# Kernel tuning notes

Measured on AMD Instinct MI355X. Metric: run time of the kernel, lower is better.

The kernel has to match this reference:

```python
import jax, jax.numpy as jnp
import numpy as np

N, C, E = 50000, 64, 800000
EPS = 1e-5

def _ln(h, g, b):
    mu = jnp.mean(h, axis=-1, keepdims=True)
    var = jnp.var(h, axis=-1, keepdims=True)
    return (h - mu) * jax.lax.rsqrt(var + EPS) * g + b

def setup_inputs() -> dict:
    key = jax.random.key(0)
    ks = jax.random.split(key, 16)
    def w(k, i, o):
        return jax.random.normal(k, (i, o), jnp.float32) * (1.0 / np.sqrt(i))
    return {
        "x": jax.random.normal(ks[0], (N, C), jnp.float32),
        "edge_index": jax.random.randint(ks[1], (2, E), 0, N, jnp.int32),
        # structure_predictor: Linear(2C,256) -> LN(256) -> GELU -> Dropout(eval) -> Linear(256,1)
        "sp_w1": w(ks[2], 2 * C, 256), "sp_b1": jnp.zeros((256,), jnp.float32),
        "sp_g": jnp.ones((256,), jnp.float32), "sp_be": jnp.zeros((256,), jnp.float32),
        "sp_w2": w(ks[3], 256, 1), "sp_b2": jnp.zeros((1,), jnp.float32),
        # feature_reconstructor: Linear(C,2C) -> LN(2C) -> GELU -> Dropout(eval) -> Linear(2C,C)
        "fr_w1": w(ks[4], C, 2 * C), "fr_b1": jnp.zeros((2 * C,), jnp.float32),
        "fr_g": jnp.ones((2 * C,), jnp.float32), "fr_be": jnp.zeros((2 * C,), jnp.float32),
        "fr_w2": w(ks[5], 2 * C, C), "fr_b2": jnp.zeros((C,), jnp.float32),
        # projection_head: Linear(C,256) -> LN(256) -> GELU -> Linear(256,128)
        "ph_w1": w(ks[6], C, 256), "ph_b1": jnp.zeros((256,), jnp.float32),
        "ph_g": jnp.ones((256,), jnp.float32), "ph_be": jnp.zeros((256,), jnp.float32),
        "ph_w2": w(ks[7], 256, 128), "ph_b2": jnp.zeros((128,), jnp.float32),
    }

def reference(x, edge_index, sp_w1, sp_b1, sp_g, sp_be, sp_w2, sp_b2,
              fr_w1, fr_b1, fr_g, fr_be, fr_w2, fr_b2,
              ph_w1, ph_b1, ph_g, ph_be, ph_w2, ph_b2):
    row, col = edge_index[0], edge_index[1]
    edge_features = jnp.concatenate([x[row], x[col]], axis=1)  # [E, 2C]
    h = _ln(edge_features @ sp_w1 + sp_b1, sp_g, sp_be)
    structure_pred = jax.nn.gelu(h, approximate=False) @ sp_w2 + sp_b2  # [E, 1]
    h = _ln(x @ fr_w1 + fr_b1, fr_g, fr_be)
    reconstructed = jax.nn.gelu(h, approximate=False) @ fr_w2 + fr_b2  # [N, C]
    h = _ln(x @ ph_w1 + ph_b1, ph_g, ph_be)
    projected = jax.nn.gelu(h, approximate=False) @ ph_w2 + ph_b2  # [N, 128]
    return (structure_pred, reconstructed, projected)
```

## Files before the change

### kernel.cpp

```cpp
#include <hip/hip_runtime.h>
#include <hip/hip_bf16.h>

typedef __attribute__((ext_vector_type(8))) short short8;
typedef __attribute__((ext_vector_type(4))) float f32x4;
typedef __attribute__((ext_vector_type(2))) float f32x2;

#define MFMA(a, b, c) __builtin_amdgcn_mfma_f32_16x16x32_bf16((a), (b), (c), 0, 0, 0)

__device__ __forceinline__ unsigned short f2bf(float f) {
    unsigned int u = __float_as_uint(f);
    u += 0x7fffu + ((u >> 16) & 1u);
    return (unsigned short)(u >> 16);
}

__device__ __forceinline__ unsigned int cvt_pk_bf16(float lo, float hi) {
    unsigned int d;
    asm("v_cvt_pk_bf16_f32 %0, %1, %2" : "=v"(d) : "v"(lo), "v"(hi));
    return d;
}

template<int CTRL>
__device__ __forceinline__ float dpp_addf(float v) {
    int t = __builtin_amdgcn_update_dpp(0, __float_as_int(v), CTRL, 0xF, 0xF, true);
    return v + __int_as_float(t);
}
__device__ __forceinline__ float rowsum16(float v) {
    v = dpp_addf<0x121>(v);
    v = dpp_addf<0x122>(v);
    v = dpp_addf<0x124>(v);
    v = dpp_addf<0x128>(v);
    return v;
}

#if __has_builtin(__builtin_amdgcn_exp2f)
#define EXP2(x) __builtin_amdgcn_exp2f(x)
#else
#define EXP2(x) __expf((x) * 0.69314718f)
#endif

__device__ __forceinline__ float gelu_fast(float x) {
    float a = x * __builtin_fmaf(x * x, 0.10295427f, 2.3021210f);
    float E = EXP2(a);
    float r = __builtin_amdgcn_rcpf(E + 1.0f);
    return __builtin_fmaf(-x, r, x);
}

__device__ __forceinline__ f32x2 gelu_fast2(f32x2 x) {
    f32x2 c1 = {2.3021210f, 2.3021210f}, c2 = {0.10295427f, 0.10295427f};
    f32x2 a = x * __builtin_elementwise_fma(x * x, c2, c1);
    f32x2 E;
    E[0] = EXP2(a[0]); E[1] = EXP2(a[1]);
    f32x2 Ep = E + (f32x2){1.f, 1.f};
    f32x2 r;
    r[0] = __builtin_amdgcn_rcpf(Ep[0]); r[1] = __builtin_amdgcn_rcpf(Ep[1]);
    return __builtin_elementwise_fma(-x, r, x);
}

__device__ __forceinline__ f32x2 unpk_bf2(unsigned int a) {
    f32x2 r;
    r[0] = __uint_as_float(a << 16);
    r[1] = __uint_as_float(a & 0xffff0000u);
    return r;
}

__device__ __forceinline__ short8 load_bfrag(const float* __restrict__ w, int k0, int n, int ldn) {
    short8 r;
#pragma unroll
    for (int u = 0; u < 8; ++u)
        r[u] = (short)f2bf(w[(k0 + u) * ldn + n]);
    return r;
}
__device__ __forceinline__ short8 load_bfrag_pk(const unsigned short* __restrict__ wp,
                                                int k0, int n, int krows) {
    return *(const short8*)&wp[(n * (krows >> 3) + (k0 >> 3)) << 3];
}

template<int N1P>
struct SmemMlp {
    unsigned short sS[64 * N1P];
    float rstat[64 * 8];
};

template<int K, int N1, int N2, int MI, bool PK>
__device__ void mlp_tile(SmemMlp<N1 + 8>& sm, const float* __restrict__ x,
                         const void* __restrict__ w1v, const float* __restrict__ b1,
                         const float* __restrict__ g, const float* __restrict__ be,
                         const void* __restrict__ w2v, const float* __restrict__ b2,
                         float* __restrict__ out, int Nrows, int t) {
    constexpr int R = MI * 16;
    constexpr int KP = K + 8, N1P = N1 + 8;
    constexpr int CPW1 = N1 / 4;
    constexpr int JT1 = CPW1 / 16;
    constexpr int KK1 = K / 32;
    constexpr int KK2 = N1 / 32;
    constexpr int JT2 = N2 / 64;
    constexpr int TPR = 256 / R;
    constexpr int FPT = K / TPR;
    constexpr int F4 = FPT / 4;

    const int tid = threadIdx.x;
    const int wave = tid >> 6, lane = tid & 63;
    const int l15 = lane & 15, quad = lane >> 4;
    const int r0 = t * R;

    {
        int m0 = tid / TPR, pp = tid % TPR;
        int rowg = r0 + m0; if (rowg >= Nrows) rowg = Nrows - 1;
        const float4* src = (const float4*)(x + (long)rowg * K + pp * FPT);
        unsigned short* dst = &sm.sS[m0 * KP + pp * FPT];
#pragma unroll
        for (int u = 0; u < F4; ++u) {
            float4 f = src[u];
            ushort4 h; h.x = f2bf(f.x); h.y = f2bf(f.y); h.z = f2bf(f.z); h.w = f2bf(f.w);
            *(ushort4*)(dst + 4 * u) = h;
        }
    }

    short8 breg1[JT1][KK1];
#pragma unroll
    for (int j = 0; j < JT1; ++j)
#pragma unroll
        for (int kk = 0; kk < KK1; ++kk) {
            int k0 = kk * 32 + quad * 8, n = CPW1 * wave + 16 * j + l15;
            if constexpr (PK) breg1[j][kk] = load_bfrag_pk((const unsigned short*)w1v, k0, n, K);
            else              breg1[j][kk] = load_bfrag((const float*)w1v, k0, n, N1);
        }

    float b1v[JT1], gv[JT1], bev[JT1];
#pragma unroll
    for (int j = 0; j < JT1; ++j) {
        int c = CPW1 * wave + 16 * j + l15;
        b1v[j] = b1[c]; gv[j] = g[c]; bev[j] = be[c];
    }
    float b2v[JT2];
#pragma unroll
    for (int j = 0; j < JT2; ++j) b2v[j] = b2[wave * 16 * JT2 + 16 * j + l15];

    __syncthreads();

    f32x4 acc1[MI][JT1];
#pragma unroll
    for (int i = 0; i < MI; ++i)
#pragma unroll
        for (int j = 0; j < JT1; ++j)
            acc1[i][j] = (f32x4){0.f, 0.f, 0.f, 0.f};

#pragma unroll
    for (int kk = 0; kk < KK1; ++kk) {
        short8 a[MI];
#pragma unroll
        for (int i = 0; i < MI; ++i)
            a[i] = *(const short8*)&sm.sS[(16 * i + l15) * KP + kk * 32 + quad * 8];
#pragma unroll
        for (int i = 0; i < MI; ++i)
#pragma unroll
            for (int j = 0; j < JT1; ++j)
                acc1[i][j] = MFMA(a[i], breg1[j][kk], acc1[i][j]);
    }

#pragma unroll
    for (int i = 0; i < MI; ++i)
#pragma unroll
        for (int r = 0; r < 4; ++r) {
            float s = 0.f, ss = 0.f;
#pragma unroll
            for (int j = 0; j < JT1; ++j) {
                float v = acc1[i][j][r] + b1v[j];
                acc1[i][j][r] = v;
                s += v; ss = __builtin_fmaf(v, v, ss);
            }
            s = rowsum16(s); ss = rowsum16(ss);
            if (l15 == 0) {
                int row = 16 * i + quad * 4 + r;
                *(float2*)&sm.rstat[row * 8 + wave * 2] = make_float2(s, ss);
            }
        }
    __syncthreads();

#pragma unroll
    for (int i = 0; i < MI; ++i)
#pragma unroll
        for (int r = 0; r < 4; ++r) {
            int row = 16 * i + quad * 4 + r;
            const float4* st = (const float4*)&sm.rstat[row * 8];
            float4 q0 = st[0], q1 = st[1];
            float s  = (q0.x + q0.z) + (q1.x + q1.z);
            float ss = (q0.y + q0.w) + (q1.y + q1.w);
            float mean = s * (1.f / (float)N1);
            float var  = __builtin_fmaf(ss, 1.f / (float)N1, -mean * mean);
            float rstd = __builtin_amdgcn_rsqf(var + 1e-5f);
            float nm = -mean * rstd;
#pragma unroll
            for (int j = 0; j < JT1; ++j) {
                float tt = __builtin_fmaf(acc1[i][j][r], rstd, nm);
                float xn = __builtin_fmaf(tt, gv[j], bev[j]);
                sm.sS[row * N1P + CPW1 * wave + 16 * j + l15] = f2bf(gelu_fast(xn));
            }
        }
    __syncthreads();

    f32x4 acc2[MI][JT2];
#pragma unroll
    for (int i = 0; i < MI; ++i)
#pragma unroll
        for (int j = 0; j < JT2; ++j)
            acc2[i][j] = (f32x4){0.f, 0.f, 0.f, 0.f};

#pragma unroll
    for (int kk = 0; kk < KK2; ++kk) {
        short8 bf[JT2];
#pragma unroll
        for (int j = 0; j < JT2; ++j) {
            int k0 = kk * 32 + quad * 8, n = wave * 16 * JT2 + 16 * j + l15;
            if constexpr (PK) bf[j] = load_bfrag_pk((const unsigned short*)w2v, k0, n, N1);
            else              bf[j] = load_bfrag((const float*)w2v, k0, n, N2);
        }
        short8 a[MI];
#pragma unroll
        for (int i = 0; i < MI; ++i)
            a[i] = *(const short8*)&sm.sS[(16 * i + l15) * N1P + kk * 32 + quad * 8];
#pragma unroll
        for (int i = 0; i < MI; ++i)
#pragma unroll
            for (int j = 0; j < JT2; ++j)
                acc2[i][j] = MFMA(a[i], bf[j], acc2[i][j]);
    }

#pragma unroll
    for (int i = 0; i < MI; ++i)
#pragma unroll
        for (int r = 0; r < 4; ++r) {
            int rowg = r0 + 16 * i + quad * 4 + r;
            if (rowg < Nrows) {
#pragma unroll
                for (int j = 0; j < JT2; ++j)
                    out[(long)rowg * N2 + wave * 16 * JT2 + 16 * j + l15] = acc2[i][j][r] + b2v[j];
            }
        }
}

template<bool PK>
__device__ void proj_tile(unsigned short* sX , const float* __restrict__ x,
                          const void* __restrict__ w1v, const float* __restrict__ b1,
                          unsigned short* __restrict__ P, int N, int tile, int isB) {
    constexpr int KP = 72;
    const int tid = threadIdx.x;
    const int wave = tid >> 6, lane = tid & 63;
    const int l15 = lane & 15, quad = lane >> 4;
    const int r0 = tile * 64;

    {
        int m0 = tid >> 2, pp = tid & 3;
        int rowg = r0 + m0; if (rowg >= N) rowg = N - 1;
        const float4* src = (const float4*)(x + (long)rowg * 64 + pp * 16);
        unsigned short* dst = &sX[m0 * KP + pp * 16];
#pragma unroll
        for (int u = 0; u < 4; ++u) {
            float4 f = src[u];
            ushort4 h; h.x = f2bf(f.x); h.y = f2bf(f.y); h.z = f2bf(f.z); h.w = f2bf(f.w);
            *(ushort4*)(dst + 4 * u) = h;
        }
    }

    short8 breg[4][2];
#pragma unroll
    for (int j = 0; j < 4; ++j)
#pragma unroll
        for (int kk = 0; kk < 2; ++kk) {
            int k0 = isB * 64 + kk * 32 + quad * 8, n = wave * 64 + 16 * j + l15;
            if constexpr (PK) breg[j][kk] = load_bfrag_pk((const unsigned short*)w1v, k0, n, 128);
            else              breg[j][kk] = load_bfrag((const float*)w1v, k0, n, 256);
        }

    float b1v[4];
#pragma unroll
    for (int j = 0; j < 4; ++j)
        b1v[j] = isB ? 0.f : b1[wave * 64 + 16 * j + l15];

    __syncthreads();

    f32x4 acc[4][4];
#pragma unroll
    for (int i = 0; i < 4; ++i)
#pragma unroll
        for (int j = 0; j < 4; ++j)
            acc[i][j] = (f32x4){0.f, 0.f, 0.f, 0.f};

#pragma unroll
    for (int kk = 0; kk < 2; ++kk) {
        short8 a[4];
#pragma unroll
        for (int i = 0; i < 4; ++i)
            a[i] = *(const short8*)&sX[(16 * i + l15) * KP + kk * 32 + quad * 8];
#pragma unroll
        for (int i = 0; i < 4; ++i)
#pragma unroll
            for (int j = 0; j < 4; ++j)
                acc[i][j] = MFMA(a[i], breg[j][kk], acc[i][j]);
    }

#pragma unroll
    for (int i = 0; i < 4; ++i)
#pragma unroll
        for (int r = 0; r < 4; ++r) {
            int rowg = r0 + 16 * i + quad * 4 + r;
            if (rowg < N) {
                uint2 d;
                d.x = cvt_pk_bf16(acc[i][0][r] + b1v[0], acc[i][1][r] + b1v[1]);
                d.y = cvt_pk_bf16(acc[i][2][r] + b1v[2], acc[i][3][r] + b1v[3]);
                *(uint2*)(P + (long)rowg * 256 + wave * 64 + l15 * 4) = d;
            }
        }
}

__device__ __forceinline__ int clamp_e(long v, int E) {
    return v < (long)E ? (int)v : E - 1;
}

__device__ void edge_role2(const unsigned short* __restrict__ Pa,
                           const unsigned short* __restrict__ Pb,
                           const int* __restrict__ ei,
                           const float* __restrict__ g, const float* __restrict__ be,
                           const float* __restrict__ w2, const float* __restrict__ b2,
                           float* __restrict__ out, int E, int ebid, int nebk) {
    const int tid = threadIdx.x;
    const int lane = tid & 63;
    const int quad = lane >> 4, l15 = lane & 15;

    f32x2 gv2[8], bev2[8], w2v2[8];
#pragma unroll
    for (int k = 0; k < 8; ++k) {
#pragma unroll
        for (int h = 0; h < 2; ++h) {
            int u = 2 * k + h;
            int c = ((l15 >> 2) << 6) + ((u & 3) << 4) + ((l15 & 3) << 2) + (u >> 2);
            gv2[k][h] = g[c]; bev2[k][h] = be[c]; w2v2[k][h] = w2[c];
        }
    }
    const float b2v = b2[0];

    const int wid = ebid * 4 + (tid >> 6);
    const long stride = (long)nebk * 16L;
    long base = (long)wid * 4;
    if (base >= E) return;

    int ir1, ic1;
    uint4 cA0, cA1, cB0, cB1;
    {
        int e0 = clamp_e(base + quad, E);
        int r = ei[e0], c = ei[E + e0];
        const uint4* pa = (const uint4*)(Pa + (long)r * 256 + l15 * 16);
        const uint4* pb = (const uint4*)(Pb + (long)c * 256 + l15 * 16);
        cA0 = pa[0]; cA1 = pa[1]; cB0 = pb[0]; cB1 = pb[1];
        int e1 = clamp_e(base + stride + quad, E);
        ir1 = ei[e1]; ic1 = ei[E + e1];
    }

    for (; base < E; base += stride) {
        int e2 = clamp_e(base + 2 * stride + quad, E);
        int ir2 = ei[e2];
        int ic2 = ei[E + e2];
        const uint4* pa = (const uint4*)(Pa + (long)ir1 * 256 + l15 * 16);
        const uint4* pb = (const uint4*)(Pb + (long)ic1 * 256 + l15 * 16);
        uint4 nA0 = pa[0], nA1 = pa[1], nB0 = pb[0], nB1 = pb[1];

        unsigned int av[8] = {cA0.x, cA0.y, cA0.z, cA0.w, cA1.x, cA1.y, cA1.z, cA1.w};
        unsigned int bv[8] = {cB0.x, cB0.y, cB0.z, cB0.w, cB1.x, cB1.y, cB1.z, cB1.w};

        f32x2 h2[8];
        f32x2 s2 = {0.f, 0.f}, ss2 = {0.f, 0.f};
#pragma unroll
        for (int k = 0; k < 8; ++k) {
            h2[k] = unpk_bf2(av[k]) + unpk_bf2(bv[k]);
            s2 = s2 + h2[k];
            ss2 = __builtin_elementwise_fma(h2[k], h2[k], ss2);
        }
        float s = s2[0] + s2[1], ss = ss2[0] + ss2[1];
        s = rowsum16(s); ss = rowsum16(ss);

        float mean = s * (1.f / 256.f);
        float var  = __builtin_fmaf(ss, 1.f / 256.f, -mean * mean);
        float rstd = __builtin_amdgcn_rsqf(var + 1e-5f);
        float nm = -mean * rstd;
        f32x2 rstd2 = {rstd, rstd}, nm2 = {nm, nm};

        f32x2 spp2 = {0.f, 0.f};
#pragma unroll
        for (int k = 0; k < 8; ++k) {
            f32x2 tt = __builtin_elementwise_fma(h2[k], rstd2, nm2);
            f32x2 xn = __builtin_elementwise_fma(tt, gv2[k], bev2[k]);
            spp2 = __builtin_elementwise_fma(gelu_fast2(xn), w2v2[k], spp2);
        }
        float spp = rowsum16(spp2[0] + spp2[1]);
        long eL = base + quad;
        if (l15 == 0 && eL < E) out[eL] = spp + b2v;

        cA0 = nA0; cA1 = nA1; cB0 = nB0; cB1 = nB1;
        ir1 = ir2; ic1 = ic2;
    }
}

__global__ __launch_bounds__(256)
void repack_kernel(const float* __restrict__ sp_w1, const float* __restrict__ fr_w1,
                   const float* __restrict__ fr_w2, const float* __restrict__ ph_w1,
                   const float* __restrict__ ph_w2, unsigned short* __restrict__ wp) {
    int e = blockIdx.x * 256 + threadIdx.x;
    const float* src; unsigned short* dst; int K, Nn;
    if (e < 32768)      { src = sp_w1; dst = wp;         K = 128; Nn = 256; }
    else if (e < 40960) { src = fr_w1; dst = wp + 32768; K = 64;  Nn = 128; e -= 32768; }
    else if (e < 49152) { src = fr_w2; dst = wp + 40960; K = 128; Nn = 64;  e -= 40960; }
    else if (e < 65536) { src = ph_w1; dst = wp + 49152; K = 64;  Nn = 256; e -= 49152; }
    else if (e < 98304) { src = ph_w2; dst = wp + 65536; K = 256; Nn = 128; e -= 65536; }
    else return;
    int n = e / K, k = e % K;
    dst[(n * (K >> 3) + (k >> 3)) * 8 + (k & 7)] = f2bf(src[k * Nn + n]);
}

union SmemPrep {
    unsigned short sX[64 * 72];
    SmemMlp<136> a;
    SmemMlp<264> b;
};

template<bool PK>
__global__ __launch_bounds__(256)
void prep_kernel(const float* __restrict__ x,
                 const void* __restrict__ sp_w1, const float* __restrict__ sp_b1,
                 const void* __restrict__ fr_w1, const float* __restrict__ fr_b1,
                 const float* __restrict__ fr_g, const float* __restrict__ fr_be,
                 const void* __restrict__ fr_w2, const float* __restrict__ fr_b2,
                 const void* __restrict__ ph_w1, const float* __restrict__ ph_b1,
                 const float* __restrict__ ph_g, const float* __restrict__ ph_be,
                 const void* __restrict__ ph_w2, const float* __restrict__ ph_b2,
                 unsigned short* __restrict__ Pa, unsigned short* __restrict__ Pb,
                 float* __restrict__ out_rec, float* __restrict__ out_proj,
                 int N, int ntN, int nFR, int nPH) {
    __shared__ SmemPrep sm;
    const int b = blockIdx.x;
    if (b < nPH) {
        mlp_tile<64, 256, 128, 2, PK>(sm.b, x, ph_w1, ph_b1, ph_g, ph_be, ph_w2, ph_b2,
                                      out_proj, N, b);
    } else if (b < nPH + nFR) {
        mlp_tile<64, 128, 64, 4, PK>(sm.a, x, fr_w1, fr_b1, fr_g, fr_be, fr_w2, fr_b2,
                                     out_rec, N, b - nPH);
    } else {
        int q = b - nPH - nFR;
        int isB = q >= ntN;
        int tile = isB ? q - ntN : q;
        proj_tile<PK>(sm.sX, x, sp_w1, sp_b1, isB ? Pb : Pa, N, tile, isB);
    }
}

__global__ __launch_bounds__(256)
void edge_stream(const unsigned short* __restrict__ Pa, const unsigned short* __restrict__ Pb,
                 const int* __restrict__ ei,
                 const float* __restrict__ g, const float* __restrict__ be,
                 const float* __restrict__ w2, const float* __restrict__ b2,
                 float* __restrict__ out, int E) {
    edge_role2(Pa, Pb, ei, g, be, w2, b2, out, E, blockIdx.x, gridDim.x);
}

struct SmemEdge {
    unsigned short sA[2][32 * 136];
    float rstat[32 * 8];
    float spL[32 * 4];
};
union SmemU {
    SmemEdge e;
    SmemMlp<136> a;
    SmemMlp<264> b;
};

__device__ void edge_role(SmemEdge& sm, const float* __restrict__ x, const int* __restrict__ ei,
                          const float* __restrict__ w1, const float* __restrict__ b1,
                          const float* __restrict__ g, const float* __restrict__ be,
                          const float* __restrict__ w2, const float* __restrict__ b2,
                          float* __restrict__ out, int E, int bid, int nblocks) {
    constexpr int KP = 136;
    const int tid = threadIdx.x;
    const int cw = tid >> 6, lane = tid & 63;
    const int l15 = lane & 15, quad = lane >> 4;

    short8 breg[4][4];
#pragma unroll
    for (int j = 0; j < 4; ++j)
#pragma unroll
        for (int kk = 0; kk < 4; ++kk)
            breg[j][kk] = load_bfrag(w1, kk * 32 + quad * 8, cw * 64 + 16 * j + l15, 256);

    float b1v[4], gv[4], bev[4], w2v[4];
#pragma unroll
    for (int j = 0; j < 4; ++j) {
        int c = cw * 64 + 16 * j + l15;
        b1v[j] = b1[c]; gv[j] = g[c]; bev[j] = be[c]; w2v[j] = w2[c];
    }
    const float b2v = b2[0];

    const int ntiles = (E + 31) >> 5;
    const int eLoc = tid >> 3, p = tid & 7;
    const int node = p >> 2, foff = (p & 3) * 16;

    float4 pf[4];
    auto issue = [&](int t) {
        int e = t * 32 + eLoc; if (e >= E) e = E - 1;
        int idx = ei[node * E + e];
        const float4* src = (const float4*)(x + (long)idx * 64 + foff);
#pragma unroll
        for (int u = 0; u < 4; ++u) pf[u] = src[u];
    };
    auto stage = [&](int buf) {
        unsigned short* dst = &sm.sA[buf][eLoc * KP + node * 64 + foff];
#pragma unroll
        for (int u = 0; u < 4; ++u) {
            ushort4 h;
            h.x = f2bf(pf[u].x); h.y = f2bf(pf[u].y);
            h.z = f2bf(pf[u].z); h.w = f2bf(pf[u].w);
            *(ushort4*)(dst + 4 * u) = h;
        }
    };

    int t = bid;
    if (t >= ntiles) return;
    issue(t); stage(0);
    if (t + nblocks < ntiles) issue(t + nblocks);
    __syncthreads();
    int cur = 0;

    for (; t < ntiles; t += nblocks) {
        f32x4 acc[2][4];
#pragma unroll
        for (int i = 0; i < 2; ++i)
#pragma unroll
            for (int j = 0; j < 4; ++j)
                acc[i][j] = (f32x4){0.f, 0.f, 0.f, 0.f};

#pragma unroll
        for (int kk = 0; kk < 4; ++kk) {
            short8 a[2];
#pragma unroll
            for (int i = 0; i < 2; ++i)
                a[i] = *(const short8*)&sm.sA[cur][(16 * i + l15) * KP + kk * 32 + quad * 8];
#pragma unroll
            for (int i = 0; i < 2; ++i)
#pragma unroll
                for (int j = 0; j < 4; ++j)
                    acc[i][j] = MFMA(a[i], breg[j][kk], acc[i][j]);
        }

        if (t + nblocks < ntiles) {
            stage(cur ^ 1);
            if (t + 2 * nblocks < ntiles) issue(t + 2 * nblocks);
        }

#pragma unroll
        for (int i = 0; i < 2; ++i)
#pragma unroll
            for (int r = 0; r < 4; ++r) {
                float v0 = acc[i][0][r] + b1v[0];
                float v1 = acc[i][1][r] + b1v[1];
                float v2 = acc[i][2][r] + b1v[2];
                float v3 = acc[i][3][r] + b1v[3];
                acc[i][0][r] = v0; acc[i][1][r] = v1; acc[i][2][r] = v2; acc[i][3][r] = v3;
                float s  = (v0 + v1) + (v2 + v3);
                float ss = __builtin_fmaf(v0, v0, __builtin_fmaf(v1, v1,
                           __builtin_fmaf(v2, v2, v3 * v3)));
                s = rowsum16(s); ss = rowsum16(ss);
                if (l15 == 0) {
                    int row = 16 * i + quad * 4 + r;
                    *(float2*)&sm.rstat[row * 8 + cw * 2] = make_float2(s, ss);
                }
            }
        __syncthreads();

#pragma unroll
        for (int i = 0; i < 2; ++i)
#pragma unroll
            for (int r = 0; r < 4; ++r) {
                int row = 16 * i + quad * 4 + r;
                const float4* st = (const float4*)&sm.rstat[row * 8];
                float4 q0 = st[0], q1 = st[1];
                float s  = (q0.x + q0.z) + (q1.x + q1.z);
                float ss = (q0.y + q0.w) + (q1.y + q1.w);
                float mean = s * (1.f / 256.f);
                float var  = __builtin_fmaf(ss, 1.f / 256.f, -mean * mean);
                float rstd = __builtin_amdgcn_rsqf(var + 1e-5f);
                float nm = -mean * rstd;
                float spp = 0.f;
#pragma unroll
                for (int j = 0; j < 4; ++j) {
                    float tt = __builtin_fmaf(acc[i][j][r], rstd, nm);
                    float xn = __builtin_fmaf(tt, gv[j], bev[j]);
                    spp = __builtin_fmaf(gelu_fast(xn), w2v[j], spp);
                }
                spp = rowsum16(spp);
                if (l15 == 0) sm.spL[row * 4 + cw] = spp;
            }
        __syncthreads();

        if (tid < 32) {
            int e = t * 32 + tid;
            if (e < E) {
                const float4* sp = (const float4*)&sm.spL[tid * 4];
                float4 u0 = sp[0];
                out[e] = ((u0.x + u0.y) + (u0.z + u0.w)) + b2v;
            }
        }
        cur ^= 1;
    }
}

__global__ __launch_bounds__(256, 3)
void fused_all(const float* __restrict__ x, const int* __restrict__ ei,
               const float* __restrict__ sp_w1, const float* __restrict__ sp_b1,
               const float* __restrict__ sp_g, const float* __restrict__ sp_be,
               const float* __restrict__ sp_w2, const float* __restrict__ sp_b2,
               const float* __restrict__ fr_w1, const float* __restrict__ fr_b1,
               const float* __restrict__ fr_g, const float* __restrict__ fr_be,
               const float* __restrict__ fr_w2, const float* __restrict__ fr_b2,
               const float* __restrict__ ph_w1, const float* __restrict__ ph_b1,
               const float* __restrict__ ph_g, const float* __restrict__ ph_be,
               const float* __restrict__ ph_w2, const float* __restrict__ ph_b2,
               float* __restrict__ out_sp, float* __restrict__ out_rec,
               float* __restrict__ out_proj, int N, int E) {
    __shared__ SmemU sm;
    const int b = blockIdx.x;
    if (b < 128) {
        for (int tt = b; tt < (N + 63) / 64; tt += 128) {
            __syncthreads();
            mlp_tile<64, 128, 64, 4, false>(sm.a, x, fr_w1, fr_b1, fr_g, fr_be, fr_w2, fr_b2,
                                            out_rec, N, tt);
        }
    } else if (b < 256) {
        for (int tt = b - 128; tt < (N + 31) / 32; tt += 128) {
            __syncthreads();
            mlp_tile<64, 256, 128, 2, false>(sm.b, x, ph_w1, ph_b1, ph_g, ph_be, ph_w2, ph_b2,
                                             out_proj, N, tt);
        }
    } else {
        edge_role(sm.e, x, ei, sp_w1, sp_b1, sp_g, sp_be, sp_w2, sp_b2,
                  out_sp, E, b - 256, 1024);
    }
}

extern "C" void kernel_launch(void* const* d_in, const int* in_sizes, int n_in,
                              void* d_out, int out_size, void* d_ws, size_t ws_size,
                              hipStream_t stream) {
    const float* x     = (const float*)d_in[0];
    const int*   ei    = (const int*)d_in[1];
    const float* sp_w1 = (const float*)d_in[2];
    const float* sp_b1 = (const float*)d_in[3];
    const float* sp_g  = (const float*)d_in[4];
    const float* sp_be = (const float*)d_in[5];
    const float* sp_w2 = (const float*)d_in[6];
    const float* sp_b2 = (const float*)d_in[7];
    const float* fr_w1 = (const float*)d_in[8];
    const float* fr_b1 = (const float*)d_in[9];
    const float* fr_g  = (const float*)d_in[10];
    const float* fr_be = (const float*)d_in[11];
    const float* fr_w2 = (const float*)d_in[12];
    const float* fr_b2 = (const float*)d_in[13];
    const float* ph_w1 = (const float*)d_in[14];
    const float* ph_b1 = (const float*)d_in[15];
    const float* ph_g  = (const float*)d_in[16];
    const float* ph_be = (const float*)d_in[17];
    const float* ph_w2 = (const float*)d_in[18];
    const float* ph_b2 = (const float*)d_in[19];

    const int N = in_sizes[0] / 64;
    const int E = in_sizes[1] / 2;

    float* out_sp   = (float*)d_out;
    float* out_rec  = out_sp + E;
    float* out_proj = out_rec + (size_t)N * 64;

    const size_t pbytes  = 2ull * (size_t)N * 256 * sizeof(unsigned short);
    const size_t wbytes  = 98304 * sizeof(unsigned short);
    const size_t needed  = pbytes;
    const size_t needed2 = pbytes + wbytes;

    const int ntN = (N + 63) / 64;
    const int nFR = (N + 63) / 64;
    const int nPH = (N + 31) / 32;

    if (ws_size >= needed2) {
        unsigned short* wp = (unsigned short*)d_ws;
        unsigned short* Pa = wp + 98304;
        unsigned short* Pb = Pa + (size_t)N * 256;
        const unsigned short* wp_sp  = wp;
        const unsigned short* wp_fr1 = wp + 32768;
        const unsigned short* wp_fr2 = wp + 40960;
        const unsigned short* wp_ph1 = wp + 49152;
        const unsigned short* wp_ph2 = wp + 65536;

        repack_kernel<<<dim3(384), dim3(256), 0, stream>>>(
            sp_w1, fr_w1, fr_w2, ph_w1, ph_w2, wp);

        prep_kernel<true><<<dim3(nPH + nFR + 2 * ntN), dim3(256), 0, stream>>>(
            x, wp_sp, sp_b1,
            wp_fr1, fr_b1, fr_g, fr_be, wp_fr2, fr_b2,
            wp_ph1, ph_b1, ph_g, ph_be, wp_ph2, ph_b2,
            Pa, Pb, out_rec, out_proj, N, ntN, nFR, nPH);

        edge_stream<<<dim3(2048), dim3(256), 0, stream>>>(
            Pa, Pb, ei, sp_g, sp_be, sp_w2, sp_b2, out_sp, E);
    } else if (ws_size >= needed) {
        unsigned short* Pa = (unsigned short*)d_ws;
        unsigned short* Pb = Pa + (size_t)N * 256;

        prep_kernel<false><<<dim3(nPH + nFR + 2 * ntN), dim3(256), 0, stream>>>(
            x, sp_w1, sp_b1,
            fr_w1, fr_b1, fr_g, fr_be, fr_w2, fr_b2,
            ph_w1, ph_b1, ph_g, ph_be, ph_w2, ph_b2,
            Pa, Pb, out_rec, out_proj, N, ntN, nFR, nPH);

        edge_stream<<<dim3(2048), dim3(256), 0, stream>>>(
            Pa, Pb, ei, sp_g, sp_be, sp_w2, sp_b2, out_sp, E);
    } else {
        fused_all<<<dim3(1280), dim3(256), 0, stream>>>(
            x, ei, sp_w1, sp_b1, sp_g, sp_be, sp_w2, sp_b2,
            fr_w1, fr_b1, fr_g, fr_be, fr_w2, fr_b2,
            ph_w1, ph_b1, ph_g, ph_be, ph_w2, ph_b2,
            out_sp, out_rec, out_proj, N, E);
    }
}
```

Measured before the change: 258.3 us.

## Overlap edge streaming with node MLPs via atomic work queue in one kernel

```diff
diff --git a/kernel.cpp b/kernel.cpp
--- a/kernel.cpp
+++ b/kernel.cpp
@@ -75,14 +75,14 @@
     return *(const short8*)&wp[(n * (krows >> 3) + (k0 >> 3)) << 3];
 }
 
-template<int N1P>
+template<int R, int N1P>
 struct SmemMlp {
-    unsigned short sS[64 * N1P];
-    float rstat[64 * 8];
+    unsigned short sS[R * N1P];
+    float rstat[R * 8];
 };
 
 template<int K, int N1, int N2, int MI, bool PK>
-__device__ void mlp_tile(SmemMlp<N1 + 8>& sm, const float* __restrict__ x,
+__device__ void mlp_tile(SmemMlp<MI * 16, N1 + 8>& sm, const float* __restrict__ x,
                          const void* __restrict__ w1v, const float* __restrict__ b1,
                          const float* __restrict__ g, const float* __restrict__ be,
                          const void* __restrict__ w2v, const float* __restrict__ b2,
@@ -240,9 +240,10 @@
 }
 
 template<bool PK>
-__device__ void proj_tile(unsigned short* sX , const float* __restrict__ x,
-                          const void* __restrict__ w1v, const float* __restrict__ b1,
-                          unsigned short* __restrict__ P, int N, int tile, int isB) {
+__device__ void proj_tile2(unsigned short* sX , const float* __restrict__ x,
+                           const void* __restrict__ w1v, const float* __restrict__ b1,
+                           unsigned short* __restrict__ Pa, unsigned short* __restrict__ Pb,
+                           int N, int tile) {
     constexpr int KP = 72;
     const int tid = threadIdx.x;
     const int wave = tid >> 6, lane = tid & 63;
@@ -261,60 +262,119 @@
             *(ushort4*)(dst + 4 * u) = h;
         }
     }
-
-    short8 breg[4][2];
-#pragma unroll
-    for (int j = 0; j < 4; ++j)
+    __syncthreads();
+
+#pragma unroll 1
+    for (int isB = 0; isB < 2; ++isB) {
+        unsigned short* __restrict__ P = isB ? Pb : Pa;
+
+        short8 breg[4][2];
+#pragma unroll
+        for (int j = 0; j < 4; ++j)
+#pragma unroll
+            for (int kk = 0; kk < 2; ++kk) {
+                int k0 = isB * 64 + kk * 32 + quad * 8, n = wave * 64 + 16 * j + l15;
+                if constexpr (PK) breg[j][kk] = load_bfrag_pk((const unsigned short*)w1v, k0, n, 128);
+                else              breg[j][kk] = load_bfrag((const float*)w1v, k0, n, 256);
+            }
+
+        float b1v[4];
+#pragma unroll
+        for (int j = 0; j < 4; ++j)
+            b1v[j] = isB ? 0.f : b1[wave * 64 + 16 * j + l15];
+
+        f32x4 acc[4][4];
+#pragma unroll
+        for (int i = 0; i < 4; ++i)
+#pragma unroll
+            for (int j = 0; j < 4; ++j)
+                acc[i][j] = (f32x4){0.f, 0.f, 0.f, 0.f};
+
 #pragma unroll
         for (int kk = 0; kk < 2; ++kk) {
-            int k0 = isB * 64 + kk * 32 + quad * 8, n = wave * 64 + 16 * j + l15;
-            if constexpr (PK) breg[j][kk] = load_bfrag_pk((const unsigned short*)w1v, k0, n, 128);
-            else              breg[j][kk] = load_bfrag((const float*)w1v, k0, n, 256);
-        }
-
-    float b1v[4];
-#pragma unroll
-    for (int j = 0; j < 4; ++j)
-        b1v[j] = isB ? 0.f : b1[wave * 64 + 16 * j + l15];
-
-    __syncthreads();
-
-    f32x4 acc[4][4];
-#pragma unroll
-    for (int i = 0; i < 4; ++i)
-#pragma unroll
-        for (int j = 0; j < 4; ++j)
-            acc[i][j] = (f32x4){0.f, 0.f, 0.f, 0.f};
-
-#pragma unroll
-    for (int kk = 0; kk < 2; ++kk) {
-        short8 a[4];
+            short8 a[4];
+#pragma unroll
+            for (int i = 0; i < 4; ++i)
+                a[i] = *(const short8*)&sX[(16 * i + l15) * KP + kk * 32 + quad * 8];
+#pragma unroll
+            for (int i = 0; i < 4; ++i)
+#pragma unroll
+                for (int j = 0; j < 4; ++j)
+                    acc[i][j] = MFMA(a[i], breg[j][kk], acc[i][j]);
+        }
+
 #pragma unroll
         for (int i = 0; i < 4; ++i)
-            a[i] = *(const short8*)&sX[(16 * i + l15) * KP + kk * 32 + quad * 8];
-#pragma unroll
-        for (int i = 0; i < 4; ++i)
-#pragma unroll
-            for (int j = 0; j < 4; ++j)
-                acc[i][j] = MFMA(a[i], breg[j][kk], acc[i][j]);
-    }
-
-#pragma unroll
-    for (int i = 0; i < 4; ++i)
-#pragma unroll
-        for (int r = 0; r < 4; ++r) {
-            int rowg = r0 + 16 * i + quad * 4 + r;
-            if (rowg < N) {
-                uint2 d;
-                d.x = cvt_pk_bf16(acc[i][0][r] + b1v[0], acc[i][1][r] + b1v[1]);
-                d.y = cvt_pk_bf16(acc[i][2][r] + b1v[2], acc[i][3][r] + b1v[3]);
-                *(uint2*)(P + (long)rowg * 256 + wave * 64 + l15 * 4) = d;
+#pragma unroll
+            for (int r = 0; r < 4; ++r) {
+                int rowg = r0 + 16 * i + quad * 4 + r;
+                if (rowg < N) {
+                    uint2 d;
+                    d.x = cvt_pk_bf16(acc[i][0][r] + b1v[0], acc[i][1][r] + b1v[1]);
+                    d.y = cvt_pk_bf16(acc[i][2][r] + b1v[2], acc[i][3][r] + b1v[3]);
+                    *(uint2*)(P + (long)rowg * 256 + wave * 64 + l15 * 4) = d;
+                }
             }
-        }
+    }
 }
 
 __device__ __forceinline__ int clamp_e(long v, int E) {
     return v < (long)E ? (int)v : E - 1;
+}
+
+struct EdgeParams {
+    f32x2 gv2[8], bev2[8], w2v2[8];
+    float b2v;
+};
+
+__device__ __forceinline__ void edge_params(EdgeParams& ep, int l15,
+                                            const float* __restrict__ g,
+                                            const float* __restrict__ be,
+                                            const float* __restrict__ w2,
+                                            const float* __restrict__ b2) {
+#pragma unroll
+    for (int k = 0; k < 8; ++k) {
+#pragma unroll
+        for (int h = 0; h < 2; ++h) {
+            int u = 2 * k + h;
+            int c = ((l15 >> 2) << 6) + ((u & 3) << 4) + ((l15 & 3) << 2) + (u >> 2);
+            ep.gv2[k][h] = g[c]; ep.bev2[k][h] = be[c]; ep.w2v2[k][h] = w2[c];
+        }
+    }
+    ep.b2v = b2[0];
+}
+
+__device__ __forceinline__ float edge_compute(const EdgeParams& ep,
+                                              const uint4& cA0, const uint4& cA1,
+                                              const uint4& cB0, const uint4& cB1) {
+    unsigned int av[8] = {cA0.x, cA0.y, cA0.z, cA0.w, cA1.x, cA1.y, cA1.z, cA1.w};
+    unsigned int bv[8] = {cB0.x, cB0.y, cB0.z, cB0.w, cB1.x, cB1.y, cB1.z, cB1.w};
+
+    f32x2 h2[8];
+    f32x2 s2 = {0.f, 0.f}, ss2 = {0.f, 0.f};
+#pragma unroll
+    for (int k = 0; k < 8; ++k) {
+        h2[k] = unpk_bf2(av[k]) + unpk_bf2(bv[k]);
+        s2 = s2 + h2[k];
+        ss2 = __builtin_elementwise_fma(h2[k], h2[k], ss2);
+    }
+    float s = s2[0] + s2[1], ss = ss2[0] + ss2[1];
+    s = rowsum16(s); ss = rowsum16(ss);
+
+    float mean = s * (1.f / 256.f);
+    float var  = __builtin_fmaf(ss, 1.f / 256.f, -mean * mean);
+    float rstd = __builtin_amdgcn_rsqf(var + 1e-5f);
+    float nm = -mean * rstd;
+    f32x2 rstd2 = {rstd, rstd}, nm2 = {nm, nm};
+
+    f32x2 spp2 = {0.f, 0.f};
+#pragma unroll
+    for (int k = 0; k < 8; ++k) {
+        f32x2 tt = __builtin_elementwise_fma(h2[k], rstd2, nm2);
+        f32x2 xn = __builtin_elementwise_fma(tt, ep.gv2[k], ep.bev2[k]);
+        spp2 = __builtin_elementwise_fma(gelu_fast2(xn), ep.w2v2[k], spp2);
+    }
+    return rowsum16(spp2[0] + spp2[1]);
 }
 
 __device__ void edge_role2(const unsigned short* __restrict__ Pa,
@@ -327,17 +387,8 @@
     const int lane = tid & 63;
     const int quad = lane >> 4, l15 = lane & 15;
 
-    f32x2 gv2[8], bev2[8], w2v2[8];
-#pragma unroll
-    for (int k = 0; k < 8; ++k) {
-#pragma unroll
-        for (int h = 0; h < 2; ++h) {
-            int u = 2 * k + h;
-            int c = ((l15 >> 2) << 6) + ((u & 3) << 4) + ((l15 & 3) << 2) + (u >> 2);
-            gv2[k][h] = g[c]; bev2[k][h] = be[c]; w2v2[k][h] = w2[c];
-        }
-    }
-    const float b2v = b2[0];
+    EdgeParams ep;
+    edge_params(ep, l15, g, be, w2, b2);
 
     const int wid = ebid * 4 + (tid >> 6);
     const long stride = (long)nebk * 16L;
@@ -364,39 +415,66 @@
         const uint4* pb = (const uint4*)(Pb + (long)ic1 * 256 + l15 * 16);
         uint4 nA0 = pa[0], nA1 = pa[1], nB0 = pb[0], nB1 = pb[1];
 
-        unsigned int av[8] = {cA0.x, cA0.y, cA0.z, cA0.w, cA1.x, cA1.y, cA1.z, cA1.w};
-        unsigned int bv[8] = {cB0.x, cB0.y, cB0.z, cB0.w, cB1.x, cB1.y, cB1.z, cB1.w};
-
-        f32x2 h2[8];
-        f32x2 s2 = {0.f, 0.f}, ss2 = {0.f, 0.f};
-#pragma unroll
-        for (int k = 0; k < 8; ++k) {
-            h2[k] = unpk_bf2(av[k]) + unpk_bf2(bv[k]);
-            s2 = s2 + h2[k];
-            ss2 = __builtin_elementwise_fma(h2[k], h2[k], ss2);
-        }
-        float s = s2[0] + s2[1], ss = ss2[0] + ss2[1];
-        s = rowsum16(s); ss = rowsum16(ss);
-
-        float mean = s * (1.f / 256.f);
-        float var  = __builtin_fmaf(ss, 1.f / 256.f, -mean * mean);
-        float rstd = __builtin_amdgcn_rsqf(var + 1e-5f);
-        float nm = -mean * rstd;
-        f32x2 rstd2 = {rstd, rstd}, nm2 = {nm, nm};
-
-        f32x2 spp2 = {0.f, 0.f};
-#pragma unroll
-        for (int k = 0; k < 8; ++k) {
-            f32x2 tt = __builtin_elementwise_fma(h2[k], rstd2, nm2);
-            f32x2 xn = __builtin_elementwise_fma(tt, gv2[k], bev2[k]);
-            spp2 = __builtin_elementwise_fma(gelu_fast2(xn), w2v2[k], spp2);
-        }
-        float spp = rowsum16(spp2[0] + spp2[1]);
+        float spp = edge_compute(ep, cA0, cA1, cB0, cB1);
         long eL = base + quad;
-        if (l15 == 0 && eL < E) out[eL] = spp + b2v;
+        if (l15 == 0 && eL < E) out[eL] = spp + ep.b2v;
 
         cA0 = nA0; cA1 = nA1; cB0 = nB0; cB1 = nB1;
         ir1 = ir2; ic1 = ic2;
+    }
+}
+
+__device__ void edge_role3(const unsigned short* __restrict__ Pa,
+                           const unsigned short* __restrict__ Pb,
+                           const int* __restrict__ ei,
+                           const float* __restrict__ g, const float* __restrict__ be,
+                           const float* __restrict__ w2, const float* __restrict__ b2,
+                           float* __restrict__ out, int E,
+                           int* __restrict__ ctr, volatile int* sbc) {
+    const int tid = threadIdx.x;
+    const int lane = tid & 63;
+    const int quad = lane >> 4, l15 = lane & 15;
+    const int wave = tid >> 6;
+
+    EdgeParams ep;
+    edge_params(ep, l15, g, be, w2, b2);
+
+    for (;;) {
+        if (tid == 0) *sbc = atomicAdd(ctr, 1);
+        __syncthreads();
+        const long base0 = (long)(*sbc) * 256;
+        __syncthreads();
+        if (base0 >= E) break;
+        const long wb = base0 + wave * 64;
+
+        int ir1, ic1;
+        uint4 cA0, cA1, cB0, cB1;
+        {
+            int e0 = clamp_e(wb + quad, E);
+            int r = ei[e0], c = ei[E + e0];
+            const uint4* pa = (const uint4*)(Pa + (long)r * 256 + l15 * 16);
+            const uint4* pb = (const uint4*)(Pb + (long)c * 256 + l15 * 16);
+            cA0 = pa[0]; cA1 = pa[1]; cB0 = pb[0]; cB1 = pb[1];
+            int e1 = clamp_e(wb + 4 + quad, E);
+            ir1 = ei[e1]; ic1 = ei[E + e1];
+        }
+
+#pragma unroll 1
+        for (int i = 0; i < 16; ++i) {
+            int e2 = clamp_e(wb + (long)(i + 2) * 4 + quad, E);
+            int ir2 = ei[e2];
+            int ic2 = ei[E + e2];
+            const uint4* pa = (const uint4*)(Pa + (long)ir1 * 256 + l15 * 16);
+            const uint4* pb = (const uint4*)(Pb + (long)ic1 * 256 + l15 * 16);
+            uint4 nA0 = pa[0], nA1 = pa[1], nB0 = pb[0], nB1 = pb[1];
+
+            float spp = edge_compute(ep, cA0, cA1, cB0, cB1);
+            long eL = wb + (long)i * 4 + quad;
+            if (l15 == 0 && eL < E) out[eL] = spp + ep.b2v;
+
+            cA0 = nA0; cA1 = nA1; cB0 = nB0; cB1 = nB1;
+            ir1 = ir2; ic1 = ic2;
+        }
     }
 }
 
@@ -416,38 +494,80 @@
     dst[(n * (K >> 3) + (k >> 3)) * 8 + (k & 7)] = f2bf(src[k * Nn + n]);
 }
 
-union SmemPrep {
-    unsigned short sX[64 * 72];
-    SmemMlp<136> a;
-    SmemMlp<264> b;
+template<bool PK>
+__global__ __launch_bounds__(256, 4)
+void proj_kernel2(const float* __restrict__ x, const void* __restrict__ w1v,
+                  const float* __restrict__ b1, unsigned short* __restrict__ Pa,
+                  unsigned short* __restrict__ Pb, int N, int* __restrict__ ctr) {
+    __shared__ unsigned short sX[64 * 72];
+    if (blockIdx.x == 0 && threadIdx.x == 0) *ctr = 0;
+    proj_tile2<PK>(sX, x, w1v, b1, Pa, Pb, N, blockIdx.x);
+}
+
+union SmemMain {
+    SmemMlp<64, 136> a;
+    SmemMlp<32, 264> b;
+    int c;
 };
 
 template<bool PK>
-__global__ __launch_bounds__(256)
-void prep_kernel(const float* __restrict__ x,
-                 const void* __restrict__ sp_w1, const float* __restrict__ sp_b1,
+__global__ __launch_bounds__(256, 4)
+void main_kernel(const float* __restrict__ x, const int* __restrict__ ei,
                  const void* __restrict__ fr_w1, const float* __restrict__ fr_b1,
                  const float* __restrict__ fr_g, const float* __restrict__ fr_be,
                  const void* __restrict__ fr_w2, const float* __restrict__ fr_b2,
                  const void* __restrict__ ph_w1, const float* __restrict__ ph_b1,
                  const float* __restrict__ ph_g, const float* __restrict__ ph_be,
                  const void* __restrict__ ph_w2, const float* __restrict__ ph_b2,
-                 unsigned short* __restrict__ Pa, unsigned short* __restrict__ Pb,
-                 float* __restrict__ out_rec, float* __restrict__ out_proj,
-                 int N, int ntN, int nFR, int nPH) {
+                 const unsigned short* __restrict__ Pa, const unsigned short* __restrict__ Pb,
+                 const float* __restrict__ sp_g, const float* __restrict__ sp_be,
+                 const float* __restrict__ sp_w2, const float* __restrict__ sp_b2,
+                 float* __restrict__ out_sp, float* __restrict__ out_rec,
+                 float* __restrict__ out_proj,
+                 int N, int E, int nFR, int nPH, int* __restrict__ ctr) {
+    __shared__ SmemMain sm;
+    const int b = blockIdx.x;
+    if (b & 1) {
+        int h = b >> 1;
+        if (h < nFR)
+            mlp_tile<64, 128, 64, 4, PK>(sm.a, x, fr_w1, fr_b1, fr_g, fr_be, fr_w2, fr_b2,
+                                         out_rec, N, h);
+        else if (h < nFR + nPH)
+            mlp_tile<64, 256, 128, 2, PK>(sm.b, x, ph_w1, ph_b1, ph_g, ph_be, ph_w2, ph_b2,
+                                          out_proj, N, h - nFR);
+    } else {
+        edge_role3(Pa, Pb, ei, sp_g, sp_be, sp_w2, sp_b2, out_sp, E, ctr, &sm.c);
+    }
+}
+
+union SmemPrep {
+    unsigned short sX[64 * 72];
+    SmemMlp<64, 136> a;
+    SmemMlp<32, 264> b;
+};
+
+__global__ __launch_bounds__(256)
+void prep_fallback(const float* __restrict__ x,
+                   const float* __restrict__ sp_w1, const float* __restrict__ sp_b1,
+                   const float* __restrict__ fr_w1, const float* __restrict__ fr_b1,
+                   const float* __restrict__ fr_g, const float* __restrict__ fr_be,
+                   const float* __restrict__ fr_w2, const float* __restrict__ fr_b2,
+                   const float* __restrict__ ph_w1, const float* __restrict__ ph_b1,
+                   const float* __restrict__ ph_g, const float* __restrict__ ph_be,
+                   const float* __restrict__ ph_w2, const float* __restrict__ ph_b2,
+                   unsigned short* __restrict__ Pa, unsigned short* __restrict__ Pb,
+                   float* __restrict__ out_rec, float* __restrict__ out_proj,
+                   int N, int ntN, int nFR, int nPH) {
     __shared__ SmemPrep sm;
     const int b = blockIdx.x;
     if (b < nPH) {
-        mlp_tile<64, 256, 128, 2, PK>(sm.b, x, ph_w1, ph_b1, ph_g, ph_be, ph_w2, ph_b2,
-                                      out_proj, N, b);
+        mlp_tile<64, 256, 128, 2, false>(sm.b, x, ph_w1, ph_b1, ph_g, ph_be, ph_w2, ph_b2,
+                                         out_proj, N, b);
     } else if (b < nPH + nFR) {
-        mlp_tile<64, 128, 64, 4, PK>(sm.a, x, fr_w1, fr_b1, fr_g, fr_be, fr_w2, fr_b2,
-                                     out_rec, N, b - nPH);
+        mlp_tile<64, 128, 64, 4, false>(sm.a, x, fr_w1, fr_b1, fr_g, fr_be, fr_w2, fr_b2,
+                                        out_rec, N, b - nPH);
     } else {
-        int q = b - nPH - nFR;
-        int isB = q >= ntN;
-        int tile = isB ? q - ntN : q;
-        proj_tile<PK>(sm.sX, x, sp_w1, sp_b1, isB ? Pb : Pa, N, tile, isB);
+        proj_tile2<false>(sm.sX, x, sp_w1, sp_b1, Pa, Pb, N, b - nPH - nFR);
     }
 }
 
@@ -458,188 +578,6 @@
                  const float* __restrict__ w2, const float* __restrict__ b2,
                  float* __restrict__ out, int E) {
     edge_role2(Pa, Pb, ei, g, be, w2, b2, out, E, blockIdx.x, gridDim.x);
-}
-
-struct SmemEdge {
-    unsigned short sA[2][32 * 136];
-    float rstat[32 * 8];
-    float spL[32 * 4];
-};
-union SmemU {
-    SmemEdge e;
-    SmemMlp<136> a;
-    SmemMlp<264> b;
-};
-
-__device__ void edge_role(SmemEdge& sm, const float* __restrict__ x, const int* __restrict__ ei,
-                          const float* __restrict__ w1, const float* __restrict__ b1,
-                          const float* __restrict__ g, const float* __restrict__ be,
-                          const float* __restrict__ w2, const float* __restrict__ b2,
-                          float* __restrict__ out, int E, int bid, int nblocks) {
-    constexpr int KP = 136;
-    const int tid = threadIdx.x;
-    const int cw = tid >> 6, lane = tid & 63;
-    const int l15 = lane & 15, quad = lane >> 4;
-
-    short8 breg[4][4];
-#pragma unroll
-    for (int j = 0; j < 4; ++j)
-#pragma unroll
-        for (int kk = 0; kk < 4; ++kk)
-            breg[j][kk] = load_bfrag(w1, kk * 32 + quad * 8, cw * 64 + 16 * j + l15, 256);
-
-    float b1v[4], gv[4], bev[4], w2v[4];
-#pragma unroll
-    for (int j = 0; j < 4; ++j) {
-        int c = cw * 64 + 16 * j + l15;
-        b1v[j] = b1[c]; gv[j] = g[c]; bev[j] = be[c]; w2v[j] = w2[c];
-    }
-    const float b2v = b2[0];
-
-    const int ntiles = (E + 31) >> 5;
-    const int eLoc = tid >> 3, p = tid & 7;
-    const int node = p >> 2, foff = (p & 3) * 16;
-
-    float4 pf[4];
-    auto issue = [&](int t) {
-        int e = t * 32 + eLoc; if (e >= E) e = E - 1;
-        int idx = ei[node * E + e];
-        const float4* src = (const float4*)(x + (long)idx * 64 + foff);
-#pragma unroll
-        for (int u = 0; u < 4; ++u) pf[u] = src[u];
-    };
-    auto stage = [&](int buf) {
-        unsigned short* dst = &sm.sA[buf][eLoc * KP + node * 64 + foff];
-#pragma unroll
-        for (int u = 0; u < 4; ++u) {
-            ushort4 h;
-            h.x = f2bf(pf[u].x); h.y = f2bf(pf[u].y);
-            h.z = f2bf(pf[u].z); h.w = f2bf(pf[u].w);
-            *(ushort4*)(dst + 4 * u) = h;
-        }
-    };
-
-    int t = bid;
-    if (t >= ntiles) return;
-    issue(t); stage(0);
-    if (t + nblocks < ntiles) issue(t + nblocks);
-    __syncthreads();
-    int cur = 0;
-
-    for (; t < ntiles; t += nblocks) {
-        f32x4 acc[2][4];
-#pragma unroll
-        for (int i = 0; i < 2; ++i)
-#pragma unroll
-            for (int j = 0; j < 4; ++j)
-                acc[i][j] = (f32x4){0.f, 0.f, 0.f, 0.f};
-
-#pragma unroll
-        for (int kk = 0; kk < 4; ++kk) {
-            short8 a[2];
-#pragma unroll
-            for (int i = 0; i < 2; ++i)
-                a[i] = *(const short8*)&sm.sA[cur][(16 * i + l15) * KP + kk * 32 + quad * 8];
-#pragma unroll
-            for (int i = 0; i < 2; ++i)
-#pragma unroll
-                for (int j = 0; j < 4; ++j)
-                    acc[i][j] = MFMA(a[i], breg[j][kk], acc[i][j]);
-        }
-
-        if (t + nblocks < ntiles) {
-            stage(cur ^ 1);
-            if (t + 2 * nblocks < ntiles) issue(t + 2 * nblocks);
-        }
-
-#pragma unroll
-        for (int i = 0; i < 2; ++i)
-#pragma unroll
-            for (int r = 0; r < 4; ++r) {
-                float v0 = acc[i][0][r] + b1v[0];
-                float v1 = acc[i][1][r] + b1v[1];
-                float v2 = acc[i][2][r] + b1v[2];
-                float v3 = acc[i][3][r] + b1v[3];
-                acc[i][0][r] = v0; acc[i][1][r] = v1; acc[i][2][r] = v2; acc[i][3][r] = v3;
-                float s  = (v0 + v1) + (v2 + v3);
-                float ss = __builtin_fmaf(v0, v0, __builtin_fmaf(v1, v1,
-                           __builtin_fmaf(v2, v2, v3 * v3)));
-                s = rowsum16(s); ss = rowsum16(ss);
-                if (l15 == 0) {
-                    int row = 16 * i + quad * 4 + r;
-                    *(float2*)&sm.rstat[row * 8 + cw * 2] = make_float2(s, ss);
-                }
-            }
-        __syncthreads();
-
-#pragma unroll
-        for (int i = 0; i < 2; ++i)
-#pragma unroll
-            for (int r = 0; r < 4; ++r) {
-                int row = 16 * i + quad * 4 + r;
-                const float4* st = (const float4*)&sm.rstat[row * 8];
-                float4 q0 = st[0], q1 = st[1];
-                float s  = (q0.x + q0.z) + (q1.x + q1.z);
-                float ss = (q0.y + q0.w) + (q1.y + q1.w);
-                float mean = s * (1.f / 256.f);
-                float var  = __builtin_fmaf(ss, 1.f / 256.f, -mean * mean);
-                float rstd = __builtin_amdgcn_rsqf(var + 1e-5f);
-                float nm = -mean * rstd;
-                float spp = 0.f;
-#pragma unroll
-                for (int j = 0; j < 4; ++j) {
-                    float tt = __builtin_fmaf(acc[i][j][r], rstd, nm);
-                    float xn = __builtin_fmaf(tt, gv[j], bev[j]);
-                    spp = __builtin_fmaf(gelu_fast(xn), w2v[j], spp);
-                }
-                spp = rowsum16(spp);
-                if (l15 == 0) sm.spL[row * 4 + cw] = spp;
-            }
-        __syncthreads();
-
-        if (tid < 32) {
-            int e = t * 32 + tid;
-            if (e < E) {
-                const float4* sp = (const float4*)&sm.spL[tid * 4];
-                float4 u0 = sp[0];
-                out[e] = ((u0.x + u0.y) + (u0.z + u0.w)) + b2v;
-            }
-        }
-        cur ^= 1;
-    }
-}
-
-__global__ __launch_bounds__(256, 3)
-void fused_all(const float* __restrict__ x, const int* __restrict__ ei,
-               const float* __restrict__ sp_w1, const float* __restrict__ sp_b1,
-               const float* __restrict__ sp_g, const float* __restrict__ sp_be,
-               const float* __restrict__ sp_w2, const float* __restrict__ sp_b2,
-               const float* __restrict__ fr_w1, const float* __restrict__ fr_b1,
-               const float* __restrict__ fr_g, const float* __restrict__ fr_be,
-               const float* __restrict__ fr_w2, const float* __restrict__ fr_b2,
-               const float* __restrict__ ph_w1, const float* __restrict__ ph_b1,
-               const float* __restrict__ ph_g, const float* __restrict__ ph_be,
-               const float* __restrict__ ph_w2, const float* __restrict__ ph_b2,
-               float* __restrict__ out_sp, float* __restrict__ out_rec,
-               float* __restrict__ out_proj, int N, int E) {
-    __shared__ SmemU sm;
-    const int b = blockIdx.x;
-    if (b < 128) {
-        for (int tt = b; tt < (N + 63) / 64; tt += 128) {
-            __syncthreads();
-            mlp_tile<64, 128, 64, 4, false>(sm.a, x, fr_w1, fr_b1, fr_g, fr_be, fr_w2, fr_b2,
-                                            out_rec, N, tt);
-        }
-    } else if (b < 256) {
-        for (int tt = b - 128; tt < (N + 31) / 32; tt += 128) {
-            __syncthreads();
-            mlp_tile<64, 256, 128, 2, false>(sm.b, x, ph_w1, ph_b1, ph_g, ph_be, ph_w2, ph_b2,
-                                             out_proj, N, tt);
-        }
-    } else {
-        edge_role(sm.e, x, ei, sp_w1, sp_b1, sp_g, sp_be, sp_w2, sp_b2,
-                  out_sp, E, b - 256, 1024);
-    }
 }
 
 extern "C" void kernel_launch(void* const* d_in, const int* in_sizes, int n_in,
@@ -676,7 +614,7 @@
     const size_t pbytes  = 2ull * (size_t)N * 256 * sizeof(unsigned short);
     const size_t wbytes  = 98304 * sizeof(unsigned short);
     const size_t needed  = pbytes;
-    const size_t needed2 = pbytes + wbytes;
+    const size_t needed2 = pbytes + wbytes + 16;
 
     const int ntN = (N + 63) / 64;
     const int nFR = (N + 63) / 64;
@@ -686,6 +624,7 @@
         unsigned short* wp = (unsigned short*)d_ws;
         unsigned short* Pa = wp + 98304;
         unsigned short* Pb = Pa + (size_t)N * 256;
+        int* ctr = (int*)(Pb + (size_t)N * 256);
         const unsigned short* wp_sp  = wp;
         const unsigned short* wp_fr1 = wp + 32768;
         const unsigned short* wp_fr2 = wp + 40960;
@@ -695,19 +634,20 @@
         repack_kernel<<<dim3(384), dim3(256), 0, stream>>>(
             sp_w1, fr_w1, fr_w2, ph_w1, ph_w2, wp);
 
-        prep_kernel<true><<<dim3(nPH + nFR + 2 * ntN), dim3(256), 0, stream>>>(
-            x, wp_sp, sp_b1,
+        proj_kernel2<true><<<dim3(ntN), dim3(256), 0, stream>>>(
+            x, wp_sp, sp_b1, Pa, Pb, N, ctr);
+
+        main_kernel<true><<<dim3(2 * (nFR + nPH)), dim3(256), 0, stream>>>(
+            x, ei,
             wp_fr1, fr_b1, fr_g, fr_be, wp_fr2, fr_b2,
             wp_ph1, ph_b1, ph_g, ph_be, wp_ph2, ph_b2,
-            Pa, Pb, out_rec, out_proj, N, ntN, nFR, nPH);
-
-        edge_stream<<<dim3(2048), dim3(256), 0, stream>>>(
-            Pa, Pb, ei, sp_g, sp_be, sp_w2, sp_b2, out_sp, E);
+            Pa, Pb, sp_g, sp_be, sp_w2, sp_b2,
+            out_sp, out_rec, out_proj, N, E, nFR, nPH, ctr);
     } else if (ws_size >= needed) {
         unsigned short* Pa = (unsigned short*)d_ws;
         unsigned short* Pb = Pa + (size_t)N * 256;
 
-        prep_kernel<false><<<dim3(nPH + nFR + 2 * ntN), dim3(256), 0, stream>>>(
+        prep_fallback<<<dim3(nPH + nFR + ntN), dim3(256), 0, stream>>>(
             x, sp_w1, sp_b1,
             fr_w1, fr_b1, fr_g, fr_be, fr_w2, fr_b2,
             ph_w1, ph_b1, ph_g, ph_be, ph_w2, ph_b2,
@@ -716,10 +656,14 @@
         edge_stream<<<dim3(2048), dim3(256), 0, stream>>>(
             Pa, Pb, ei, sp_g, sp_be, sp_w2, sp_b2, out_sp, E);
     } else {
-        fused_all<<<dim3(1280), dim3(256), 0, stream>>>(
-            x, ei, sp_w1, sp_b1, sp_g, sp_be, sp_w2, sp_b2,
+        prep_fallback<<<dim3(nPH + nFR + ntN), dim3(256), 0, stream>>>(
+            x, sp_w1, sp_b1,
             fr_w1, fr_b1, fr_g, fr_be, fr_w2, fr_b2,
             ph_w1, ph_b1, ph_g, ph_be, ph_w2, ph_b2,
-            out_sp, out_rec, out_proj, N, E);
-    }
-}
+            (unsigned short*)d_ws, (unsigned short*)d_ws, out_rec, out_proj,
+            N, 0, nFR, nPH);
+        edge_stream<<<dim3(2048), dim3(256), 0, stream>>>(
+            (unsigned short*)d_ws, (unsigned short*)d_ws, ei,
+            sp_g, sp_be, sp_w2, sp_b2, out_sp, E);
+    }
+}
```

Result: slower. 341.5 us (+32.2%).
